# Optimization experiments

Hardware: AMD Instinct MI355X
Metric: run time of the kernel (lower is better)

The kernel has to match this reference:

```python
import jax, jax.numpy as jnp
import numpy as np

B, C, W, H = 4, 256, 64, 64


def setup_inputs() -> dict:
    key = jax.random.key(0)
    ks = jax.random.split(key, 10)
    s = 1.0 / np.sqrt(C)  # fan-in style scale for 1x1 conv weights
    return {
        "x": jax.random.normal(ks[0], (B, C, W, H), dtype=jnp.float32),
        "Wq": jax.random.normal(ks[1], (C, C), dtype=jnp.float32) * s,
        "bq": jax.random.normal(ks[2], (C,), dtype=jnp.float32) * 0.02,
        "Wk": jax.random.normal(ks[3], (C, C), dtype=jnp.float32) * s,
        "bk": jax.random.normal(ks[4], (C,), dtype=jnp.float32) * 0.02,
        "Wv": jax.random.normal(ks[5], (C, C), dtype=jnp.float32) * s,
        "bv": jax.random.normal(ks[6], (C,), dtype=jnp.float32) * 0.02,
        "rel_h": jax.random.normal(ks[7], (1, C, H, 1), dtype=jnp.float32),
        "rel_w": jax.random.normal(ks[8], (1, C, 1, W), dtype=jnp.float32),
        # gamma is initialized to 0 in the original; use a nonzero value so the
        # attention branch actually contributes (otherwise out == x).
        "gamma": jnp.full((1,), 0.5, dtype=jnp.float32),
    }


def reference(x, Wq, bq, Wk, bk, Wv, bv, rel_h, rel_w, gamma):
    Bz, Cc, Ww, Hh = x.shape
    N = Ww * Hh
    xf = x.reshape(Bz, Cc, N)  # [B, C, N]

    # 1x1 convs == per-pixel linear projections over channels
    q = jnp.einsum('oc,bcn->bno', Wq, xf) + bq            # [B, N, C]
    k = jnp.einsum('oc,bcn->bon', Wk, xf) + bk[:, None]   # [B, C, N]
    v = jnp.einsum('oc,bcn->bon', Wv, xf) + bv[:, None]   # [B, C, N]

    # relative position bias: (rel_h + rel_w) -> [C, N], projected by q
    pos = (rel_h + rel_w).reshape(Cc, N)                  # [C, N]
    energy = jnp.einsum('bnc,bcm->bnm', q, k) + q @ pos   # [B, N, N]

    att = jax.nn.softmax(energy, axis=-1)                 # [B, N, N]

    # out[b,c,m] = sum_n v[b,c,n] * att[b,m,n]
    out = jnp.einsum('bcn,bmn->bcm', v, att).reshape(Bz, Cc, Ww, Hh)
    return gamma * out + x
```

## Files before the change

### kernel.cpp

```cpp
#include <hip/hip_runtime.h>
#include <stdint.h>

#define N_TOK 4096
#define C_DIM 256
#define NSPLIT 2

typedef __attribute__((ext_vector_type(8))) short short8;
typedef __attribute__((ext_vector_type(8))) _Float16 half8;
typedef __attribute__((ext_vector_type(4))) float floatx4;
typedef __attribute__((ext_vector_type(4))) unsigned short ushort4v;

__device__ __forceinline__ unsigned short bf16_rne(float f) {
    union { float f; unsigned int u; } v; v.f = f;
    unsigned int u = v.u;
    unsigned int rounded = u + 0x7FFFu + ((u >> 16) & 1u);
    return (unsigned short)(rounded >> 16);
}
__device__ __forceinline__ float bf16_to_f(unsigned short h) {
    union { unsigned int u; float f; } v; v.u = ((unsigned int)h) << 16;
    return v.f;
}
__device__ __forceinline__ void split_bf16(float f, unsigned short& h, unsigned short& l) {
    h = bf16_rne(f);
    l = bf16_rne(f - bf16_to_f(h));
}
__device__ __forceinline__ unsigned short f2h(float f) {
    union { _Float16 h; unsigned short u; } v; v.h = (_Float16)f; return v.u;
}
__device__ __forceinline__ float h2f(unsigned short u) {
    union { unsigned short u; _Float16 h; } v; v.u = u; return (float)v.h;
}
__device__ __forceinline__ void g2l16(const void* g, void* l) {
    __builtin_amdgcn_global_load_lds(
        (const __attribute__((address_space(1))) void*)g,
        (__attribute__((address_space(3))) void*)l, 16, 0, 0);
}

__global__ __launch_bounds__(256) void prep_kernel(
    const float* __restrict__ x,
    const float* __restrict__ Wq, const float* __restrict__ Wk, const float* __restrict__ Wv,
    unsigned short* __restrict__ Xhi, unsigned short* __restrict__ Xlo,
    unsigned short* __restrict__ Whi, unsigned short* __restrict__ Wlo)
{
    const int t = threadIdx.x;
    if (blockIdx.x >= 1024) {
        const int pj = blockIdx.x - 1024;
        const float* W = (pj == 0) ? Wq : (pj == 1) ? Wk : Wv;
        unsigned short* dh = Whi + pj * 65536;
        unsigned short* dl = Wlo + pj * 65536;
        for (int it = 0; it < 64; it++) {
            const int idx = it * 1024 + t * 4;
            const float4 w = *(const float4*)&W[idx];
            unsigned short h0, l0, h1, l1, h2, l2, h3, l3;
            split_bf16(w.x, h0, l0); split_bf16(w.y, h1, l1);
            split_bf16(w.z, h2, l2); split_bf16(w.w, h3, l3);
            ushort4v vh; vh[0] = h0; vh[1] = h1; vh[2] = h2; vh[3] = h3;
            ushort4v vl; vl[0] = l0; vl[1] = l1; vl[2] = l2; vl[3] = l3;
            *(ushort4v*)&dh[idx] = vh;
            *(ushort4v*)&dl[idx] = vl;
        }
        return;
    }
    __shared__ float Xs[64 * 65];
    const int b  = blockIdx.x >> 8;
    const int ct = (blockIdx.x >> 6) & 3;
    const int nt = blockIdx.x & 63;
    const int c0 = ct * 64, n0 = nt * 64;
    {
        const int nch = t & 15, cr = t >> 4;
#pragma unroll
        for (int pass = 0; pass < 4; pass++) {
            const int c = pass * 16 + cr;
            const float4 v = *(const float4*)&x[((size_t)(b * C_DIM + c0 + c)) * N_TOK + n0 + nch * 4];
            float* row = &Xs[c * 65 + nch * 4];
            row[0] = v.x; row[1] = v.y; row[2] = v.z; row[3] = v.w;
        }
    }
    __syncthreads();
    {
        const int n = t >> 2, cc = t & 3;
        short8 vh0, vl0, vh1, vl1;
#pragma unroll
        for (int i = 0; i < 8; i++) {
            unsigned short h, l;
            split_bf16(Xs[(cc * 16 + i) * 65 + n], h, l);
            vh0[i] = (short)h; vl0[i] = (short)l;
        }
#pragma unroll
        for (int i = 0; i < 8; i++) {
            unsigned short h, l;
            split_bf16(Xs[(cc * 16 + 8 + i) * 65 + n], h, l);
            vh1[i] = (short)h; vl1[i] = (short)l;
        }
        const size_t off = ((size_t)b * N_TOK + n0 + n) * C_DIM + c0 + cc * 16;
        *(short8*)&Xhi[off] = vh0; *(short8*)&Xhi[off + 8] = vh1;
        *(short8*)&Xlo[off] = vl0; *(short8*)&Xlo[off + 8] = vl1;
    }
}

__global__ __launch_bounds__(256) void proj_kernel(
    const unsigned short* __restrict__ Xhi, const unsigned short* __restrict__ Xlo,
    const unsigned short* __restrict__ Whi, const unsigned short* __restrict__ Wlo,
    const float* __restrict__ bq, const float* __restrict__ bk, const float* __restrict__ bv,
    const float* __restrict__ relh, const float* __restrict__ relw,
    unsigned short* __restrict__ Qh,
    unsigned short* __restrict__ Kh,
    unsigned short* __restrict__ Vh)
{
    __shared__ unsigned short SM[20480];
    unsigned short* Ah = SM;
    unsigned short* Al = SM + 2048;
    unsigned short* Bh = SM + 4096;
    unsigned short* Bl = SM + 12288;

    const int t    = threadIdx.x;
    const int wave = t >> 6;
    const int lane = t & 63;
    const int l15  = lane & 15;
    const int quad = lane >> 4;

    const int bp   = blockIdx.x >> 6;
    const int proj = bp % 3;
    const int b    = bp / 3;
    const int n0   = (blockIdx.x & 63) * 64;

    const unsigned short* Xh = Xhi + ((size_t)b * N_TOK + n0) * C_DIM;
    const unsigned short* Xl = Xlo + ((size_t)b * N_TOK + n0) * C_DIM;
    const unsigned short* Wh = Whi + proj * 65536;
    const unsigned short* Wl = Wlo + proj * 65536;
    const float* bias = (proj == 0) ? bq : (proj == 1) ? bk : bv;
    const bool needlo = (proj < 2);

    floatx4 acc[16];
#pragma unroll
    for (int i = 0; i < 16; i++) acc[i] = (floatx4){0.f, 0.f, 0.f, 0.f};

    for (int c0 = 0; c0 < 256; c0 += 32) {
        {
            const int lr = lane >> 2, cp = lane & 3;
            const int key = (lr ^ (lr >> 2)) & 3;
            const int r = wave * 16 + lr;
            g2l16(Xh + (size_t)r * C_DIM + c0 + (cp ^ key) * 8, &Ah[wave * 512]);
            if (needlo) g2l16(Xl + (size_t)r * C_DIM + c0 + (cp ^ key) * 8, &Al[wave * 512]);
#pragma unroll
            for (int p = 0; p < 4; p++) {
                const int rb = (p * 4 + wave) * 16;
                const int rr = rb + lr;
                g2l16(Wh + (size_t)rr * 256 + c0 + (cp ^ key) * 8, &Bh[rb * 32]);
                if (needlo) g2l16(Wl + (size_t)rr * 256 + c0 + (cp ^ key) * 8, &Bl[rb * 32]);
            }
        }
        __syncthreads();

        const int akey = (l15 ^ (l15 >> 2)) & 3;
        const int arow = (wave * 16 + l15) * 32 + ((quad ^ akey) * 8);
        const short8 a_h = *(const short8*)&Ah[arow];
        short8 a_l;
        if (needlo) a_l = *(const short8*)&Al[arow];
#pragma unroll
        for (int ot = 0; ot < 16; ot++) {
            const int brow = (ot * 16 + l15) * 32 + ((quad ^ akey) * 8);
            const short8 b_h = *(const short8*)&Bh[brow];
            acc[ot] = __builtin_amdgcn_mfma_f32_16x16x32_bf16(a_h, b_h, acc[ot], 0, 0, 0);
            if (needlo) {
                const short8 b_l = *(const short8*)&Bl[brow];
                acc[ot] = __builtin_amdgcn_mfma_f32_16x16x32_bf16(a_l, b_h, acc[ot], 0, 0, 0);
                acc[ot] = __builtin_amdgcn_mfma_f32_16x16x32_bf16(a_h, b_l, acc[ot], 0, 0, 0);
            }
        }
        __syncthreads();
    }

    const int h0 = n0 >> 6;
    if (proj == 0) {
        unsigned short* Og = Qh + ((size_t)b * N_TOK + n0) * C_DIM;
#pragma unroll
        for (int ot = 0; ot < 16; ot++) {
            const int o = ot * 16 + l15;
            const float bs = bias[o];
#pragma unroll
            for (int r = 0; r < 4; r++) {
                const int nl = wave * 16 + quad * 4 + r;
                Og[(size_t)nl * C_DIM + o] = f2h(acc[ot][r] + bs);
            }
        }
    } else if (proj == 1) {
        unsigned short* Og = Kh + ((size_t)b * N_TOK + n0) * C_DIM;
#pragma unroll
        for (int ot = 0; ot < 16; ot++) {
            const int o = ot * 16 + l15;
            const float bs = bias[o];
            const float ph = relh[o * 64 + h0];
#pragma unroll
            for (int r = 0; r < 4; r++) {
                const int nl = wave * 16 + quad * 4 + r;
                Og[(size_t)nl * C_DIM + o] = f2h(acc[ot][r] + bs + ph + relw[o * 64 + nl]);
            }
        }
    } else {
        unsigned short* Vt = SM;
#pragma unroll
        for (int ot = 0; ot < 16; ot++) {
            const int o = ot * 16 + l15;
            const float bs = bias[o];
            const unsigned int u0 = (unsigned int)f2h(acc[ot][0] + bs) |
                                    ((unsigned int)f2h(acc[ot][1] + bs) << 16);
            const unsigned int u1 = (unsigned int)f2h(acc[ot][2] + bs) |
                                    ((unsigned int)f2h(acc[ot][3] + bs) << 16);
            uint2 uv; uv.x = u0; uv.y = u1;
            *(uint2*)&Vt[o * 72 + wave * 16 + quad * 4] = uv;
        }
        __syncthreads();
        const int ch   = t & 7;
        const int orow = t >> 3;
#pragma unroll
        for (int pass = 0; pass < 8; pass++) {
            const int o = pass * 32 + orow;
            const short8 vv = *(const short8*)&Vt[o * 72 + ch * 8];
            *(short8*)&Vh[((size_t)b * C_DIM + o) * N_TOK + n0 + ch * 8] = vv;
        }
    }
}

__global__ __launch_bounds__(256, 2) void flash_kernel(
    const unsigned short* __restrict__ Qg,
    const unsigned short* __restrict__ Kg,
    const unsigned short* __restrict__ Vg,
    unsigned short* __restrict__ Op,
    float* __restrict__ Lm)
{
    __shared__ unsigned short Ks[64 * 256];
    __shared__ unsigned short Vs[256 * 64];
    __shared__ unsigned short Pt[4 * 16 * 72];
    __shared__ float abuf[4][16];

    const int t    = threadIdx.x;
    const int wave = t >> 6;
    const int lane = t & 63;
    const int l15  = lane & 15;
    const int quad = lane >> 4;
    const int lk   = l15 & 7;

    const int bid = blockIdx.x;
    const int b   = bid & 3;
    const int s   = (bid >> 2) & 1;
    const int qt  = bid >> 3;

    const unsigned short* Kb = Kg + (size_t)b * N_TOK * C_DIM;
    const unsigned short* Vb = Vg + (size_t)b * C_DIM * N_TOK;

    half8 qf[8];
    const int qrow = qt * 64 + wave * 16 + l15;
    {
        const unsigned short* Qrow = Qg + ((size_t)b * N_TOK + qrow) * C_DIM;
#pragma unroll
        for (int ct = 0; ct < 8; ct++)
            qf[ct] = *(const half8*)&Qrow[ct * 32 + quad * 8];
    }

    floatx4 oacc[16];
#pragma unroll
    for (int i = 0; i < 16; i++) oacc[i] = (floatx4){0.f, 0.f, 0.f, 0.f};
    float m_i[4] = {-1e30f, -1e30f, -1e30f, -1e30f};
    float l_i[4] = {0.f, 0.f, 0.f, 0.f};

    unsigned short* Ptw = Pt + wave * 16 * 72;
    const int jbase = s * 2048;

    {
        const int lr = lane >> 5, cp = lane & 31;
#pragma unroll
        for (int p = 0; p < 8; p++) {
            const int jl = wave * 16 + p * 2 + lr;
            g2l16(Kb + (size_t)(jbase + jl) * C_DIM + (cp ^ (jl & 7)) * 8,
                  &Ks[(wave * 16 + p * 2) * 256]);
        }
    }

    for (int ti = 0; ti < 32; ti++) {
        const int j0 = jbase + ti * 64;

        __syncthreads();

        {
            const int lr = lane >> 3, cp = lane & 7;
#pragma unroll
            for (int p = 0; p < 8; p++) {
                const int ob = (p * 4 + wave) * 8;
                const int o  = ob + lr;
                g2l16(Vb + (size_t)o * N_TOK + j0 + (cp ^ (o & 7)) * 8, &Vs[ob * 64]);
            }
        }

        floatx4 sv[4];
#pragma unroll
        for (int jt = 0; jt < 4; jt++) {
            floatx4 a = (floatx4){0.f, 0.f, 0.f, 0.f};
#pragma unroll
            for (int ct = 0; ct < 8; ct++) {
                const half8 kb = *(const half8*)&Ks[(jt * 16 + l15) * 256 + (((ct * 4 + quad) ^ lk) * 8)];
                a = __builtin_amdgcn_mfma_f32_16x16x32_f16(qf[ct], kb, a, 0, 0, 0);
            }
            sv[jt] = a;
        }

        float alpha[4];
#pragma unroll
        for (int r = 0; r < 4; r++) {
            float mx = fmaxf(fmaxf(sv[0][r], sv[1][r]), fmaxf(sv[2][r], sv[3][r]));
            mx = fmaxf(mx, __shfl_xor(mx, 1));
            mx = fmaxf(mx, __shfl_xor(mx, 2));
            mx = fmaxf(mx, __shfl_xor(mx, 4));
            mx = fmaxf(mx, __shfl_xor(mx, 8));
            const float mn = fmaxf(m_i[r], mx);
            alpha[r] = __expf(m_i[r] - mn);
            m_i[r] = mn;
            float ps = 0.f;
#pragma unroll
            for (int jt = 0; jt < 4; jt++) {
                const float p = __expf(sv[jt][r] - mn);
                sv[jt][r] = p;
                ps += p;
            }
            ps += __shfl_xor(ps, 1);
            ps += __shfl_xor(ps, 2);
            ps += __shfl_xor(ps, 4);
            ps += __shfl_xor(ps, 8);
            l_i[r] = l_i[r] * alpha[r] + ps;
        }

#pragma unroll
        for (int jt = 0; jt < 4; jt++) {
#pragma unroll
            for (int r = 0; r < 4; r++)
                Ptw[(quad * 4 + r) * 72 + jt * 16 + l15] = f2h(sv[jt][r]);
        }
        if (l15 == 0)
            *(float4*)&abuf[wave][quad * 4] = make_float4(alpha[0], alpha[1], alpha[2], alpha[3]);
        const half8 pf0 = *(const half8*)&Ptw[l15 * 72 + quad * 8];
        const half8 pf1 = *(const half8*)&Ptw[l15 * 72 + 32 + quad * 8];
        const float am = abuf[wave][l15];
#pragma unroll
        for (int ot = 0; ot < 16; ot++) {
            oacc[ot][0] *= am; oacc[ot][1] *= am; oacc[ot][2] *= am; oacc[ot][3] *= am;
        }

        __syncthreads();

        if (ti < 31) {
            const int lr = lane >> 5, cp = lane & 31;
#pragma unroll
            for (int p = 0; p < 8; p++) {
                const int jl = wave * 16 + p * 2 + lr;
                g2l16(Kb + (size_t)(j0 + 64 + jl) * C_DIM + (cp ^ (jl & 7)) * 8,
                      &Ks[(wave * 16 + p * 2) * 256]);
            }
        }

#pragma unroll
        for (int ot = 0; ot < 16; ot++) {
            const int row = (ot * 16 + l15) * 64;
            const half8 av0 = *(const half8*)&Vs[row + ((quad ^ lk) * 8)];
            const half8 av1 = *(const half8*)&Vs[row + (((4 + quad) ^ lk) * 8)];
            oacc[ot] = __builtin_amdgcn_mfma_f32_16x16x32_f16(av0, pf0, oacc[ot], 0, 0, 0);
            oacc[ot] = __builtin_amdgcn_mfma_f32_16x16x32_f16(av1, pf1, oacc[ot], 0, 0, 0);
        }
    }

    unsigned short* Ob = Op + ((size_t)(s * 4 + b) * C_DIM) * N_TOK;
    const int n = qt * 64 + wave * 16 + l15;
#pragma unroll
    for (int ot = 0; ot < 16; ot++) {
#pragma unroll
        for (int r = 0; r < 4; r++) {
            const int c = ot * 16 + quad * 4 + r;
            Ob[(size_t)c * N_TOK + n] = f2h(oacc[ot][r]);
        }
    }
    if (l15 == 0) {
        const size_t nb = (size_t)(s * 4 + b) * N_TOK + qt * 64 + wave * 16 + quad * 4;
#pragma unroll
        for (int r = 0; r < 4; r++)
            *(float2*)&Lm[(nb + r) * 2] = make_float2(m_i[r], l_i[r]);
    }
}

__global__ __launch_bounds__(256) void merge_kernel(
    const unsigned short* __restrict__ Op,
    const float* __restrict__ Lm,
    const float* __restrict__ x,
    const float* __restrict__ gamma,
    float* __restrict__ out)
{
    const int blk = blockIdx.x;
    const int b   = blk >> 10;
    const int c   = (blk >> 2) & 255;
    const int nq  = blk & 3;
    const int n0  = nq * 1024 + threadIdx.x * 4;

    const size_t NEo = (size_t)4 * C_DIM * N_TOK;
    const size_t obase = ((size_t)b * C_DIM + c) * N_TOK + n0;

    float ms[NSPLIT][4], ls[NSPLIT][4], os[NSPLIT][4];
#pragma unroll
    for (int s = 0; s < NSPLIT; s++) {
        const uint2 u = *(const uint2*)&Op[s * NEo + obase];
        os[s][0] = h2f((unsigned short)(u.x & 0xffff));
        os[s][1] = h2f((unsigned short)(u.x >> 16));
        os[s][2] = h2f((unsigned short)(u.y & 0xffff));
        os[s][3] = h2f((unsigned short)(u.y >> 16));
        const float* Lms = Lm + (size_t)(s * 4 + b) * N_TOK * 2;
        const float4 A0 = *(const float4*)&Lms[n0 * 2];
        const float4 A1 = *(const float4*)&Lms[n0 * 2 + 4];
        ms[s][0] = A0.x; ls[s][0] = A0.y;
        ms[s][1] = A0.z; ls[s][1] = A0.w;
        ms[s][2] = A1.x; ls[s][2] = A1.y;
        ms[s][3] = A1.z; ls[s][3] = A1.w;
    }
    const float4 xv = *(const float4*)&x[obase];
    const float xin[4] = {xv.x, xv.y, xv.z, xv.w};
    const float g = gamma[0];

    float4 res;
    float* rp = (float*)&res;
#pragma unroll
    for (int i = 0; i < 4; i++) {
        float M = ms[0][i];
#pragma unroll
        for (int s = 1; s < NSPLIT; s++) M = fmaxf(M, ms[s][i]);
        float osum = 0.f, lsum = 0.f;
#pragma unroll
        for (int s = 0; s < NSPLIT; s++) {
            const float w = __expf(ms[s][i] - M);
            osum += w * os[s][i];
            lsum += w * ls[s][i];
        }
        rp[i] = g * osum / lsum + xin[i];
    }
    *(float4*)&out[obase] = res;
}

extern "C" void kernel_launch(void* const* d_in, const int* in_sizes, int n_in,
                              void* d_out, int out_size, void* d_ws, size_t ws_size,
                              hipStream_t stream) {
    const float* x     = (const float*)d_in[0];
    const float* Wq    = (const float*)d_in[1];
    const float* bq    = (const float*)d_in[2];
    const float* Wk    = (const float*)d_in[3];
    const float* bk    = (const float*)d_in[4];
    const float* Wv    = (const float*)d_in[5];
    const float* bv    = (const float*)d_in[6];
    const float* relh  = (const float*)d_in[7];
    const float* relw  = (const float*)d_in[8];
    const float* gamma = (const float*)d_in[9];
    float* out = (float*)d_out;

    const size_t NE = (size_t)4 * N_TOK * C_DIM;

    unsigned short* Op  = (unsigned short*)d_ws;
    unsigned short* Xhi = Op;
    unsigned short* Xlo = Op + NE;
    unsigned short* Whi = Op + (size_t)NSPLIT * NE;
    unsigned short* Wlo = Whi + 3 * 65536;
    unsigned short* Qh  = Wlo + 3 * 65536;
    unsigned short* Kh  = Qh + NE;
    unsigned short* Vh  = Kh + NE;
    float* Lm = (float*)(Vh + NE);

    hipLaunchKernelGGL(prep_kernel, dim3(1027), dim3(256), 0, stream,
                       x, Wq, Wk, Wv, Xhi, Xlo, Whi, Wlo);
    hipLaunchKernelGGL(proj_kernel, dim3(768), dim3(256), 0, stream,
                       Xhi, Xlo, Whi, Wlo, bq, bk, bv, relh, relw, Qh, Kh, Vh);
    hipLaunchKernelGGL(flash_kernel, dim3(512), dim3(256), 0, stream,
                       Qh, Kh, Vh, Op, Lm);
    hipLaunchKernelGGL(merge_kernel, dim3(4096), dim3(256), 0, stream,
                       Op, Lm, x, gamma, out);
}
```

Baseline: 264.1 us.

## Transpose QK MFMA, keep P in registers, widen blocks and KV splits

The QK^T MFMA operand order is swapped so each lane holds one query row's scores. That turns the row max and sum into cross-quad shuffles and removes the per-row LDS round trip for P and alpha, since P fragments are rebuilt with lane shuffles. The flash kernel is templated so that, when the workspace is large enough, it runs 8-wave blocks of 128 query rows with a 4-way KV split and half the iterations per block. The merge kernel handles 4 partials. s_setprio is raised around the MFMA loops. In exchange there are more partial outputs to write and merge, and more register pressure per block.

```diff
diff --git a/kernel.cpp b/kernel.cpp
--- a/kernel.cpp
+++ b/kernel.cpp
@@ -3,7 +3,6 @@
 
 #define N_TOK 4096
 #define C_DIM 256
-#define NSPLIT 2
 
 typedef __attribute__((ext_vector_type(8))) short short8;
 typedef __attribute__((ext_vector_type(8))) _Float16 half8;
@@ -29,6 +28,11 @@
 }
 __device__ __forceinline__ float h2f(unsigned short u) {
     union { unsigned short u; _Float16 h; } v; v.u = u; return (float)v.h;
+}
+__device__ __forceinline__ unsigned int pack2h(float a, float b) {
+    union { _Float16 h[2]; unsigned int u; } v;
+    v.h[0] = (_Float16)a; v.h[1] = (_Float16)b;
+    return v.u;
 }
 __device__ __forceinline__ void g2l16(const void* g, void* l) {
     __builtin_amdgcn_global_load_lds(
@@ -222,17 +226,21 @@
     }
 }
 
-__global__ __launch_bounds__(256, 2) void flash_kernel(
+template<int WPB, int NITER>
+__global__ __launch_bounds__(WPB * 64, WPB / 2) void flash_kernel(
     const unsigned short* __restrict__ Qg,
     const unsigned short* __restrict__ Kg,
     const unsigned short* __restrict__ Vg,
     unsigned short* __restrict__ Op,
     float* __restrict__ Lm)
 {
+    static_assert(WPB == 4 || WPB == 8, "WPB");
+    constexpr int NS    = N_TOK / (NITER * 64);
+    constexpr int QTILE = WPB * 16;
+    constexpr int QSH   = (NS == 4) ? 4 : 3;
+
     __shared__ unsigned short Ks[64 * 256];
     __shared__ unsigned short Vs[256 * 64];
-    __shared__ unsigned short Pt[4 * 16 * 72];
-    __shared__ float abuf[4][16];
 
     const int t    = threadIdx.x;
     const int wave = t >> 6;
@@ -243,14 +251,14 @@
 
     const int bid = blockIdx.x;
     const int b   = bid & 3;
-    const int s   = (bid >> 2) & 1;
-    const int qt  = bid >> 3;
+    const int s   = (bid >> 2) & (NS - 1);
+    const int qt  = bid >> QSH;
 
     const unsigned short* Kb = Kg + (size_t)b * N_TOK * C_DIM;
     const unsigned short* Vb = Vg + (size_t)b * C_DIM * N_TOK;
 
     half8 qf[8];
-    const int qrow = qt * 64 + wave * 16 + l15;
+    const int qrow = qt * QTILE + wave * 16 + l15;
     {
         const unsigned short* Qrow = Qg + ((size_t)b * N_TOK + qrow) * C_DIM;
 #pragma unroll
@@ -261,23 +269,25 @@
     floatx4 oacc[16];
 #pragma unroll
     for (int i = 0; i < 16; i++) oacc[i] = (floatx4){0.f, 0.f, 0.f, 0.f};
-    float m_i[4] = {-1e30f, -1e30f, -1e30f, -1e30f};
-    float l_i[4] = {0.f, 0.f, 0.f, 0.f};
-
-    unsigned short* Ptw = Pt + wave * 16 * 72;
-    const int jbase = s * 2048;
+    float m_i = -1e30f;
+    float l_i = 0.f;
+
+    const int jbase = s * (NITER * 64);
+    const int oddq  = quad & 1;
+    const int hiq   = quad >> 1;
+    const int own   = (quad == 0) | (quad == 3);
 
     {
         const int lr = lane >> 5, cp = lane & 31;
 #pragma unroll
-        for (int p = 0; p < 8; p++) {
-            const int jl = wave * 16 + p * 2 + lr;
+        for (int p = 0; p < 64 / WPB / 2; p++) {
+            const int jl = wave * (64 / WPB) + p * 2 + lr;
             g2l16(Kb + (size_t)(jbase + jl) * C_DIM + (cp ^ (jl & 7)) * 8,
-                  &Ks[(wave * 16 + p * 2) * 256]);
-        }
-    }
-
-    for (int ti = 0; ti < 32; ti++) {
+                  &Ks[(wave * (64 / WPB) + p * 2) * 256]);
+        }
+    }
+
+    for (int ti = 0; ti < NITER; ti++) {
         const int j0 = jbase + ti * 64;
 
         __syncthreads();
@@ -285,78 +295,121 @@
         {
             const int lr = lane >> 3, cp = lane & 7;
 #pragma unroll
-            for (int p = 0; p < 8; p++) {
-                const int ob = (p * 4 + wave) * 8;
+            for (int p = 0; p < 32 / WPB; p++) {
+                const int ob = (p * WPB + wave) * 8;
                 const int o  = ob + lr;
                 g2l16(Vb + (size_t)o * N_TOK + j0 + (cp ^ (o & 7)) * 8, &Vs[ob * 64]);
             }
         }
 
         floatx4 sv[4];
+        __builtin_amdgcn_s_setprio(1);
 #pragma unroll
         for (int jt = 0; jt < 4; jt++) {
             floatx4 a = (floatx4){0.f, 0.f, 0.f, 0.f};
 #pragma unroll
             for (int ct = 0; ct < 8; ct++) {
                 const half8 kb = *(const half8*)&Ks[(jt * 16 + l15) * 256 + (((ct * 4 + quad) ^ lk) * 8)];
-                a = __builtin_amdgcn_mfma_f32_16x16x32_f16(qf[ct], kb, a, 0, 0, 0);
+                a = __builtin_amdgcn_mfma_f32_16x16x32_f16(kb, qf[ct], a, 0, 0, 0);
             }
             sv[jt] = a;
         }
-
-        float alpha[4];
-#pragma unroll
-        for (int r = 0; r < 4; r++) {
-            float mx = fmaxf(fmaxf(sv[0][r], sv[1][r]), fmaxf(sv[2][r], sv[3][r]));
-            mx = fmaxf(mx, __shfl_xor(mx, 1));
-            mx = fmaxf(mx, __shfl_xor(mx, 2));
-            mx = fmaxf(mx, __shfl_xor(mx, 4));
-            mx = fmaxf(mx, __shfl_xor(mx, 8));
-            const float mn = fmaxf(m_i[r], mx);
-            alpha[r] = __expf(m_i[r] - mn);
-            m_i[r] = mn;
-            float ps = 0.f;
-#pragma unroll
-            for (int jt = 0; jt < 4; jt++) {
+        __builtin_amdgcn_s_setprio(0);
+
+        float mx;
+        {
+            const float a0 = fmaxf(fmaxf(sv[0][0], sv[0][1]), fmaxf(sv[0][2], sv[0][3]));
+            const float a1 = fmaxf(fmaxf(sv[1][0], sv[1][1]), fmaxf(sv[1][2], sv[1][3]));
+            const float a2 = fmaxf(fmaxf(sv[2][0], sv[2][1]), fmaxf(sv[2][2], sv[2][3]));
+            const float a3 = fmaxf(fmaxf(sv[3][0], sv[3][1]), fmaxf(sv[3][2], sv[3][3]));
+            mx = fmaxf(fmaxf(a0, a1), fmaxf(a2, a3));
+        }
+        mx = fmaxf(mx, __shfl_xor(mx, 16));
+        mx = fmaxf(mx, __shfl_xor(mx, 32));
+        const float mn    = fmaxf(m_i, mx);
+        const float alpha = __expf(m_i - mn);
+        m_i = mn;
+        float ps = 0.f;
+#pragma unroll
+        for (int jt = 0; jt < 4; jt++) {
+#pragma unroll
+            for (int r = 0; r < 4; r++) {
                 const float p = __expf(sv[jt][r] - mn);
                 sv[jt][r] = p;
                 ps += p;
             }
-            ps += __shfl_xor(ps, 1);
-            ps += __shfl_xor(ps, 2);
-            ps += __shfl_xor(ps, 4);
-            ps += __shfl_xor(ps, 8);
-            l_i[r] = l_i[r] * alpha[r] + ps;
-        }
-
-#pragma unroll
-        for (int jt = 0; jt < 4; jt++) {
-#pragma unroll
-            for (int r = 0; r < 4; r++)
-                Ptw[(quad * 4 + r) * 72 + jt * 16 + l15] = f2h(sv[jt][r]);
-        }
-        if (l15 == 0)
-            *(float4*)&abuf[wave][quad * 4] = make_float4(alpha[0], alpha[1], alpha[2], alpha[3]);
-        const half8 pf0 = *(const half8*)&Ptw[l15 * 72 + quad * 8];
-        const half8 pf1 = *(const half8*)&Ptw[l15 * 72 + 32 + quad * 8];
-        const float am = abuf[wave][l15];
+        }
+        l_i = l_i * alpha + ps;
+
+        half8 pf0, pf1;
+        {
+            const unsigned int u00 = pack2h(sv[0][0], sv[0][1]);
+            const unsigned int u01 = pack2h(sv[0][2], sv[0][3]);
+            const unsigned int u10 = pack2h(sv[1][0], sv[1][1]);
+            const unsigned int u11 = pack2h(sv[1][2], sv[1][3]);
+            const unsigned int t00 = __shfl_xor(u00, 16), t01 = __shfl_xor(u01, 16);
+            const unsigned int t10 = __shfl_xor(u10, 16), t11 = __shfl_xor(u11, 16);
+            const unsigned int L00 = oddq ? t00 : u00, H00 = oddq ? u00 : t00;
+            const unsigned int L01 = oddq ? t01 : u01, H01 = oddq ? u01 : t01;
+            const unsigned int L10 = oddq ? t10 : u10, H10 = oddq ? u10 : t10;
+            const unsigned int L11 = oddq ? t11 : u11, H11 = oddq ? u11 : t11;
+            const unsigned int ke0 = hiq ? L10 : L00, se0 = hiq ? L00 : L10;
+            const unsigned int ke1 = hiq ? L11 : L01, se1 = hiq ? L01 : L11;
+            const unsigned int ko0 = hiq ? H10 : H00, so0 = hiq ? H00 : H10;
+            const unsigned int ko1 = hiq ? H11 : H01, so1 = hiq ? H01 : H11;
+            const unsigned int re0 = __shfl_xor(se0, 32), re1 = __shfl_xor(se1, 32);
+            const unsigned int ro0 = __shfl_xor(so0, 32), ro1 = __shfl_xor(so1, 32);
+            union { unsigned int u[4]; half8 h; } pk;
+            pk.u[0] = own ? ke0 : re0;
+            pk.u[1] = own ? ke1 : re1;
+            pk.u[2] = own ? ko0 : ro0;
+            pk.u[3] = own ? ko1 : ro1;
+            pf0 = pk.h;
+        }
+        {
+            const unsigned int u00 = pack2h(sv[2][0], sv[2][1]);
+            const unsigned int u01 = pack2h(sv[2][2], sv[2][3]);
+            const unsigned int u10 = pack2h(sv[3][0], sv[3][1]);
+            const unsigned int u11 = pack2h(sv[3][2], sv[3][3]);
+            const unsigned int t00 = __shfl_xor(u00, 16), t01 = __shfl_xor(u01, 16);
+            const unsigned int t10 = __shfl_xor(u10, 16), t11 = __shfl_xor(u11, 16);
+            const unsigned int L00 = oddq ? t00 : u00, H00 = oddq ? u00 : t00;
+            const unsigned int L01 = oddq ? t01 : u01, H01 = oddq ? u01 : t01;
+            const unsigned int L10 = oddq ? t10 : u10, H10 = oddq ? u10 : t10;
+            const unsigned int L11 = oddq ? t11 : u11, H11 = oddq ? u11 : t11;
+            const unsigned int ke0 = hiq ? L10 : L00, se0 = hiq ? L00 : L10;
+            const unsigned int ke1 = hiq ? L11 : L01, se1 = hiq ? L01 : L11;
+            const unsigned int ko0 = hiq ? H10 : H00, so0 = hiq ? H00 : H10;
+            const unsigned int ko1 = hiq ? H11 : H01, so1 = hiq ? H01 : H11;
+            const unsigned int re0 = __shfl_xor(se0, 32), re1 = __shfl_xor(se1, 32);
+            const unsigned int ro0 = __shfl_xor(so0, 32), ro1 = __shfl_xor(so1, 32);
+            union { unsigned int u[4]; half8 h; } pk;
+            pk.u[0] = own ? ke0 : re0;
+            pk.u[1] = own ? ke1 : re1;
+            pk.u[2] = own ? ko0 : ro0;
+            pk.u[3] = own ? ko1 : ro1;
+            pf1 = pk.h;
+        }
+
 #pragma unroll
         for (int ot = 0; ot < 16; ot++) {
-            oacc[ot][0] *= am; oacc[ot][1] *= am; oacc[ot][2] *= am; oacc[ot][3] *= am;
+            oacc[ot][0] *= alpha; oacc[ot][1] *= alpha;
+            oacc[ot][2] *= alpha; oacc[ot][3] *= alpha;
         }
 
         __syncthreads();
 
-        if (ti < 31) {
+        if (ti < NITER - 1) {
             const int lr = lane >> 5, cp = lane & 31;
 #pragma unroll
-            for (int p = 0; p < 8; p++) {
-                const int jl = wave * 16 + p * 2 + lr;
+            for (int p = 0; p < 64 / WPB / 2; p++) {
+                const int jl = wave * (64 / WPB) + p * 2 + lr;
                 g2l16(Kb + (size_t)(j0 + 64 + jl) * C_DIM + (cp ^ (jl & 7)) * 8,
-                      &Ks[(wave * 16 + p * 2) * 256]);
-            }
-        }
-
+                      &Ks[(wave * (64 / WPB) + p * 2) * 256]);
+            }
+        }
+
+        __builtin_amdgcn_s_setprio(1);
 #pragma unroll
         for (int ot = 0; ot < 16; ot++) {
             const int row = (ot * 16 + l15) * 64;
@@ -365,10 +418,11 @@
             oacc[ot] = __builtin_amdgcn_mfma_f32_16x16x32_f16(av0, pf0, oacc[ot], 0, 0, 0);
             oacc[ot] = __builtin_amdgcn_mfma_f32_16x16x32_f16(av1, pf1, oacc[ot], 0, 0, 0);
         }
+        __builtin_amdgcn_s_setprio(0);
     }
 
     unsigned short* Ob = Op + ((size_t)(s * 4 + b) * C_DIM) * N_TOK;
-    const int n = qt * 64 + wave * 16 + l15;
+    const int n = qt * QTILE + wave * 16 + l15;
 #pragma unroll
     for (int ot = 0; ot < 16; ot++) {
 #pragma unroll
@@ -377,14 +431,16 @@
             Ob[(size_t)c * N_TOK + n] = f2h(oacc[ot][r]);
         }
     }
-    if (l15 == 0) {
-        const size_t nb = (size_t)(s * 4 + b) * N_TOK + qt * 64 + wave * 16 + quad * 4;
-#pragma unroll
-        for (int r = 0; r < 4; r++)
-            *(float2*)&Lm[(nb + r) * 2] = make_float2(m_i[r], l_i[r]);
-    }
-}
-
+    float lt = l_i;
+    lt += __shfl_xor(lt, 16);
+    lt += __shfl_xor(lt, 32);
+    if (quad == 0) {
+        const size_t nb = (size_t)(s * 4 + b) * N_TOK + n;
+        *(float2*)&Lm[nb * 2] = make_float2(m_i, lt);
+    }
+}
+
+template<int NS>
 __global__ __launch_bounds__(256) void merge_kernel(
     const unsigned short* __restrict__ Op,
     const float* __restrict__ Lm,
@@ -401,9 +457,9 @@
     const size_t NEo = (size_t)4 * C_DIM * N_TOK;
     const size_t obase = ((size_t)b * C_DIM + c) * N_TOK + n0;
 
-    float ms[NSPLIT][4], ls[NSPLIT][4], os[NSPLIT][4];
-#pragma unroll
-    for (int s = 0; s < NSPLIT; s++) {
+    float ms[NS][4], ls[NS][4], os[NS][4];
+#pragma unroll
+    for (int s = 0; s < NS; s++) {
         const uint2 u = *(const uint2*)&Op[s * NEo + obase];
         os[s][0] = h2f((unsigned short)(u.x & 0xffff));
         os[s][1] = h2f((unsigned short)(u.x >> 16));
@@ -427,10 +483,10 @@
     for (int i = 0; i < 4; i++) {
         float M = ms[0][i];
 #pragma unroll
-        for (int s = 1; s < NSPLIT; s++) M = fmaxf(M, ms[s][i]);
+        for (int s = 1; s < NS; s++) M = fmaxf(M, ms[s][i]);
         float osum = 0.f, lsum = 0.f;
 #pragma unroll
-        for (int s = 0; s < NSPLIT; s++) {
+        for (int s = 0; s < NS; s++) {
             const float w = __expf(ms[s][i] - M);
             osum += w * os[s][i];
             lsum += w * ls[s][i];
@@ -457,10 +513,13 @@
 
     const size_t NE = (size_t)4 * N_TOK * C_DIM;
 
+    const size_t need4 = ((size_t)7 * NE + 6 * 65536) * 2 + (size_t)4 * 4 * N_TOK * 2 * 4;
+    const int NS = (ws_size >= need4) ? 4 : 2;
+
     unsigned short* Op  = (unsigned short*)d_ws;
     unsigned short* Xhi = Op;
     unsigned short* Xlo = Op + NE;
-    unsigned short* Whi = Op + (size_t)NSPLIT * NE;
+    unsigned short* Whi = Op + (size_t)NS * NE;
     unsigned short* Wlo = Whi + 3 * 65536;
     unsigned short* Qh  = Wlo + 3 * 65536;
     unsigned short* Kh  = Qh + NE;
@@ -471,8 +530,15 @@
                        x, Wq, Wk, Wv, Xhi, Xlo, Whi, Wlo);
     hipLaunchKernelGGL(proj_kernel, dim3(768), dim3(256), 0, stream,
                        Xhi, Xlo, Whi, Wlo, bq, bk, bv, relh, relw, Qh, Kh, Vh);
-    hipLaunchKernelGGL(flash_kernel, dim3(512), dim3(256), 0, stream,
-                       Qh, Kh, Vh, Op, Lm);
-    hipLaunchKernelGGL(merge_kernel, dim3(4096), dim3(256), 0, stream,
-                       Op, Lm, x, gamma, out);
-}
+    if (NS == 4) {
+        hipLaunchKernelGGL((flash_kernel<8, 16>), dim3(512), dim3(512), 0, stream,
+                           Qh, Kh, Vh, Op, Lm);
+        hipLaunchKernelGGL((merge_kernel<4>), dim3(4096), dim3(256), 0, stream,
+                           Op, Lm, x, gamma, out);
+    } else {
+        hipLaunchKernelGGL((flash_kernel<4, 32>), dim3(512), dim3(256), 0, stream,
+                           Qh, Kh, Vh, Op, Lm);
+        hipLaunchKernelGGL((merge_kernel<2>), dim3(4096), dim3(256), 0, stream,
+                           Op, Lm, x, gamma, out);
+    }
+}
```

Result: slower. 401.6 us (+52.0%).
